# Kernel optimization log

Measured on AMD Instinct MI355X. Metric: run time of the kernel, lower is better.

The kernel has to match this reference:

```python
import jax, jax.numpy as jnp
import numpy as np

H = 512          # hidden_size of the active GRU_with_GCC
IN = 2048        # input_size of stream 1 (the encoded stream)
FS = 1536        # feats_size of stream 0 (auxiliary GCC stream)
B, T = 128, 64


def setup_inputs() -> dict:
    key = jax.random.key(0)
    ks = jax.random.split(key, 8)
    stdv = 1.0 / np.sqrt(H)
    u = lambda k, shape: jax.random.uniform(k, shape, jnp.float32, -stdv, stdv)
    return {
        "feat0": jax.random.normal(ks[0], (B, T, FS), jnp.float32),
        "feat1": jax.random.normal(ks[1], (B, T, IN), jnp.float32),
        "W_ih": u(ks[2], (3 * H, IN)),
        "b_ih": u(ks[3], (3 * H,)),
        "W_hh": u(ks[4], (3 * H, H)),
        "b_hh": u(ks[5], (3 * H,)),
        "W_fh": u(ks[6], (2 * H, FS)),
        "b_fh": u(ks[7], (2 * H,)),
    }


def reference(feat0, feat1, W_ih, b_ih, W_hh, b_hh, W_fh, b_fh):
    # Encoder_Baseline (eval mode -> dropout is identity), skip_info=[1,0]:
    # only stream 1 is encoded by GRU_with_GCC with feat0 as auxiliary gating.
    # Precompute input and auxiliary projections for all timesteps (batched GEMM).
    gi = jnp.einsum('bti,gi->btg', feat1, W_ih) + b_ih   # [B,T,3H]
    gf = jnp.einsum('btf,gf->btg', feat0, W_fh) + b_fh   # [B,T,2H]

    def step(h, inp):
        gi_t, gf_t = inp                                  # [B,3H], [B,2H]
        gh = h @ W_hh.T + b_hh                            # [B,3H]
        i_r, i_i, i_n = jnp.split(gi_t, 3, axis=-1)
        h_r, h_i, h_n = jnp.split(gh, 3, axis=-1)
        f_r, f_i = jnp.split(gf_t, 2, axis=-1)
        resetgate = jax.nn.sigmoid(i_r + h_r + f_r)
        inputgate = jax.nn.sigmoid(i_i + h_i + f_i)
        newgate = jnp.tanh(i_n + resetgate * h_n)
        hy = newgate + inputgate * (h - newgate)
        return hy, hy

    h0 = jnp.zeros((feat1.shape[0], H), feat1.dtype)
    hT, ys = jax.lax.scan(step, h0, (gi.transpose(1, 0, 2), gf.transpose(1, 0, 2)))
    eo = ys.transpose(1, 0, 2)                            # [B,T,H]
    return eo, hT
```

## Files before the change

kernel.cpp:

```cpp
#include <hip/hip_runtime.h>
#include <cstdint>
#include <cstddef>

typedef __bf16 bf16_t;
typedef bf16_t bf16x8 __attribute__((ext_vector_type(8)));
typedef float floatx4 __attribute__((ext_vector_type(4)));
typedef unsigned long long u64;

#define B_   128
#define T_   64
#define H_   512
#define IN_  2048
#define FS_  1536
#define M_   (B_ * T_)
#define GB_  64

__device__ __forceinline__ void async16(void* lds, const void* gp) {
  __builtin_amdgcn_global_load_lds(
      (const __attribute__((address_space(1))) void*)gp,
      (__attribute__((address_space(3))) void*)lds, 16, 0, 0);
}

__device__ __forceinline__ u64 cload64(const u64* p) {
  return __hip_atomic_load((u64*)p, __ATOMIC_RELAXED, __HIP_MEMORY_SCOPE_AGENT);
}
__device__ __forceinline__ void cstore64(u64* p, u64 v) {
  __hip_atomic_store(p, v, __ATOMIC_RELAXED, __HIP_MEMORY_SCOPE_AGENT);
}
__device__ __forceinline__ int cloadi(const int* p) {
  return __hip_atomic_load((int*)p, __ATOMIC_RELAXED, __HIP_MEMORY_SCOPE_AGENT);
}
__device__ __forceinline__ void cstorei(int* p, int v) {
  __hip_atomic_store(p, v, __ATOMIC_RELAXED, __HIP_MEMORY_SCOPE_AGENT);
}

__device__ __forceinline__ float fsigmoid(float x) {
  return __builtin_amdgcn_rcpf(1.f + __expf(-x));
}
__device__ __forceinline__ float ftanh(float x) {
  return 2.f * __builtin_amdgcn_rcpf(1.f + __expf(-2.f * x)) - 1.f;
}

__global__ __launch_bounds__(256) void cvt_bf16_k(const float* __restrict__ s,
                                                  bf16_t* __restrict__ d, int n8) {
  int i = blockIdx.x * 256 + threadIdx.x;
  if (i >= n8) return;
  const float4* s4 = (const float4*)s;
  float4 v0 = s4[2 * (size_t)i];
  float4 v1 = s4[2 * (size_t)i + 1];
  bf16x8 o;
  o[0] = (bf16_t)v0.x; o[1] = (bf16_t)v0.y; o[2] = (bf16_t)v0.z; o[3] = (bf16_t)v0.w;
  o[4] = (bf16_t)v1.x; o[5] = (bf16_t)v1.y; o[6] = (bf16_t)v1.z; o[7] = (bf16_t)v1.w;
  *(bf16x8*)(d + (size_t)i * 8) = o;
}

#define BM 128
#define BN 128
#define BK 32

__global__ __launch_bounds__(256) void gemm_bt_bias(
    const bf16_t* __restrict__ A, const bf16_t* __restrict__ B,
    const float* __restrict__ bias, float* __restrict__ C,
    int M, int N, int K) {
  __shared__ __align__(16) bf16_t As[BM * BK];
  __shared__ __align__(16) bf16_t Bs[BN * BK];

  const int tid  = threadIdx.x;
  const int lane = tid & 63;
  const int wave = tid >> 6;
  const int wr = wave >> 1, wc = wave & 1;
  const int mblk = blockIdx.y * BM;
  const int nblk = blockIdx.x * BN;

  const int sr = lane >> 2;
  const int sc = (lane & 3) * 8;
  const int c0 = wave * 2;

  const bf16_t* Ag0 = A + (size_t)(mblk + c0 * 16 + sr) * K + sc;
  const bf16_t* Ag1 = A + (size_t)(mblk + c0 * 16 + 16 + sr) * K + sc;
  const bf16_t* Bg0 = B + (size_t)(nblk + c0 * 16 + sr) * K + sc;
  const bf16_t* Bg1 = B + (size_t)(nblk + c0 * 16 + 16 + sr) * K + sc;
  bf16_t* As0 = As + c0 * 512;
  bf16_t* Bs0 = Bs + c0 * 512;

  floatx4 acc[4][4] = {};

  const int fm = lane & 15;
  const int fk = (lane >> 4) * 8;

  for (int kt = 0; kt < K; kt += BK) {
    async16(As0,       Ag0 + kt);
    async16(As0 + 512, Ag1 + kt);
    async16(Bs0,       Bg0 + kt);
    async16(Bs0 + 512, Bg1 + kt);
    __syncthreads();

    bf16x8 a[4], b[4];
#pragma unroll
    for (int i = 0; i < 4; i++)
      a[i] = *(const bf16x8*)(As + (wr * 64 + i * 16 + fm) * BK + fk);
#pragma unroll
    for (int j = 0; j < 4; j++)
      b[j] = *(const bf16x8*)(Bs + (wc * 64 + j * 16 + fm) * BK + fk);
#pragma unroll
    for (int i = 0; i < 4; i++)
#pragma unroll
      for (int j = 0; j < 4; j++)
        acc[i][j] = __builtin_amdgcn_mfma_f32_16x16x32_bf16(a[i], b[j], acc[i][j], 0, 0, 0);
    __syncthreads();
  }

  const int en  = nblk + wc * 64 + (lane & 15);
  const int em0 = mblk + wr * 64 + (lane >> 4) * 4;
#pragma unroll
  for (int j = 0; j < 4; j++) {
    int col = en + j * 16;
    float bv = bias[col];
#pragma unroll
    for (int i = 0; i < 4; i++) {
#pragma unroll
      for (int r = 0; r < 4; r++) {
        int row = em0 + i * 16 + r;
        C[(size_t)row * N + col] = acc[i][j][r] + bv;
      }
    }
  }
}

__global__ __launch_bounds__(256) void gru_scan(
    const float* __restrict__ Whh_f,
    const float* __restrict__ bhh,
    const float* __restrict__ gi,
    const float* __restrict__ gf,
    bf16_t* __restrict__ hbuf,
    int* __restrict__ flg,
    float* __restrict__ out) {
  __shared__ __align__(16) bf16_t wlds[48 * 64 * 8];
  __shared__ __align__(16) bf16_t swp[4][256];

  const int tid  = threadIdx.x;
  const int lane = tid & 63;
  const int w    = tid >> 6;
  const int lm   = lane & 15;
  const int lq   = lane >> 4;
  const int c    = blockIdx.x >> 1;
  const int mh   = blockIdx.x & 1;
  const int n0   = c * 16;

  for (int f = w; f < 48; f += 4) {
    int g = f >> 4, kt = f & 15;
    const float* src = Whh_f + (size_t)(g * H_ + n0 + lm) * H_ + kt * 32 + lq * 8;
    float4 v0 = *(const float4*)src;
    float4 v1 = *(const float4*)(src + 4);
    bf16x8 o;
    o[0] = (bf16_t)v0.x; o[1] = (bf16_t)v0.y; o[2] = (bf16_t)v0.z; o[3] = (bf16_t)v0.w;
    o[4] = (bf16_t)v1.x; o[5] = (bf16_t)v1.y; o[6] = (bf16_t)v1.z; o[7] = (bf16_t)v1.w;
    *(bf16x8*)(wlds + (f * 64 + lane) * 8) = o;
  }

  {
    u64* z = (u64*)(hbuf + (((size_t)mh * 32 + c) * 64 + w * 16) * 16) + lane;
    cstore64(z, 0ull);
  }
  asm volatile("s_waitcnt vmcnt(0)" ::: "memory");
  if (lane == 0) cstorei(flg + ((mh * 32 + c) * 4 + w) * 16, 1);
  __syncthreads();

  const float b0 = bhh[n0 + lm];
  const float b1 = bhh[H_ + n0 + lm];
  const float b2 = bhh[2 * H_ + n0 + lm];

  const int m0 = mh * 64 + w * 16;
  float hp[4] = {0.f, 0.f, 0.f, 0.f};

  float pir[4], pii[4], pin[4], pfr[4], pfi[4];
  auto prefetch = [&](int t) {
#pragma unroll
    for (int r = 0; r < 4; ++r) {
      size_t mrow = (size_t)(m0 + lq * 4 + r) * T_ + t;
      const float* gip = gi + mrow * (3 * H_) + n0 + lm;
      pir[r] = gip[0];
      pii[r] = gip[H_];
      pin[r] = gip[2 * H_];
      const float* gfp = gf + mrow * (2 * H_) + n0 + lm;
      pfr[r] = gfp[0];
      pfi[r] = gfp[H_];
    }
  };
  prefetch(0);

  const int* fpoll = flg + ((mh * 32 + (lane & 31)) * 4 + w) * 16;
  int* fme = flg + ((mh * 32 + c) * 4 + w) * 16;

  const size_t habase = ((size_t)mh * 32 * 64 + (size_t)w * 16 + lm) * 16 + (lq & 1) * 8;
  const size_t hct    = (size_t)(lq >> 1) * 64 * 16;

  for (int t = 0; t < T_; ++t) {
    for (;;) {
      int f = cloadi(fpoll);
      if (__all(f >= t + 1)) break;
      __builtin_amdgcn_s_sleep(1);
    }

    const bf16_t* hpar = hbuf + (size_t)(t & 1) * 65536;
    union { u64 u[2]; bf16x8 v; } a[16];
#pragma unroll
    for (int kt = 0; kt < 16; ++kt) {
      const u64* ap = (const u64*)(hpar + habase + hct + (size_t)kt * 2048);
      a[kt].u[0] = cload64(ap);
      a[kt].u[1] = cload64(ap + 1);
    }

    floatx4 acc[3] = {};
#pragma unroll
    for (int g = 0; g < 3; ++g)
#pragma unroll
      for (int kt = 0; kt < 16; ++kt) {
        bf16x8 b = *(const bf16x8*)(wlds + ((g * 16 + kt) * 64 + lane) * 8);
        acc[g] = __builtin_amdgcn_mfma_f32_16x16x32_bf16(a[kt].v, b, acc[g], 0, 0, 0);
      }

#pragma unroll
    for (int r = 0; r < 4; ++r) {
      int brow = m0 + lq * 4 + r;
      size_t mrow = (size_t)brow * T_ + t;
      float rg = fsigmoid(pir[r] + acc[0][r] + b0 + pfr[r]);
      float ig = fsigmoid(pii[r] + acc[1][r] + b1 + pfi[r]);
      float ng = ftanh(pin[r] + rg * (acc[2][r] + b2));
      float hy = ng + ig * (hp[r] - ng);
      hp[r] = hy;

      out[mrow * H_ + n0 + lm] = hy;
      if (t == T_ - 1)
        out[(size_t)M_ * H_ + (size_t)brow * H_ + n0 + lm] = hy;
      swp[w][(lq * 4 + r) * 16 + lm] = (bf16_t)hy;
    }

    if (t + 1 < T_) {
      asm volatile("s_waitcnt lgkmcnt(0)" ::: "memory");
      u64 pk = *(const u64*)(&swp[w][0] + lane * 4);
      bf16_t* hnxt = hbuf + (size_t)((t + 1) & 1) * 65536;
      u64* dst = (u64*)(hnxt + (((size_t)mh * 32 + c) * 64 + w * 16) * 16) + lane;
      cstore64(dst, pk);
      asm volatile("s_waitcnt vmcnt(0)" ::: "memory");
      if (lane == 0) cstorei(fme, t + 2);
      prefetch(t + 1);
    }
  }
}

extern "C" void kernel_launch(void* const* d_in, const int* in_sizes, int n_in,
                              void* d_out, int out_size, void* d_ws, size_t ws_size,
                              hipStream_t stream) {
  const float* feat0 = (const float*)d_in[0];
  const float* feat1 = (const float*)d_in[1];
  const float* W_ih  = (const float*)d_in[2];
  const float* b_ih  = (const float*)d_in[3];
  const float* W_hh  = (const float*)d_in[4];
  const float* b_hh  = (const float*)d_in[5];
  const float* W_fh  = (const float*)d_in[6];
  const float* b_fh  = (const float*)d_in[7];
  float* out = (float*)d_out;

  char* p = (char*)d_ws;
  int*    flg  = (int*)p;    p += 16384;
  bf16_t* hbuf = (bf16_t*)p; p += 2 * 65536 * 2;
  float*  gi   = (float*)p;  p += (size_t)M_ * 3 * H_ * 4;
  float*  gf   = (float*)p;  p += (size_t)M_ * 2 * H_ * 4;
  bf16_t* A1   = (bf16_t*)p; p += (size_t)M_ * IN_ * 2;
  bf16_t* A0   = (bf16_t*)p; p += (size_t)M_ * FS_ * 2;
  bf16_t* Wihb = (bf16_t*)p; p += (size_t)3 * H_ * IN_ * 2;
  bf16_t* Wfhb = (bf16_t*)p; p += (size_t)2 * H_ * FS_ * 2;

  hipMemsetAsync(flg, 0, 16384, stream);

  auto cvt = [&](const float* s, bf16_t* d, size_t n) {
    int n8 = (int)(n / 8);
    cvt_bf16_k<<<(n8 + 255) / 256, 256, 0, stream>>>(s, d, n8);
  };
  cvt(feat1, A1, (size_t)M_ * IN_);
  cvt(feat0, A0, (size_t)M_ * FS_);
  cvt(W_ih, Wihb, (size_t)3 * H_ * IN_);
  cvt(W_fh, Wfhb, (size_t)2 * H_ * FS_);

  gemm_bt_bias<<<dim3((3 * H_) / BN, M_ / BM), 256, 0, stream>>>(
      A1, Wihb, b_ih, gi, M_, 3 * H_, IN_);
  gemm_bt_bias<<<dim3((2 * H_) / BN, M_ / BM), 256, 0, stream>>>(
      A0, Wfhb, b_fh, gf, M_, 2 * H_, FS_);

  gru_scan<<<GB_, 256, 0, stream>>>(W_hh, b_hh, gi, gf, hbuf, flg, out);
}
```

Before: 549.8 us.

## Replace flag-based inter-block sync with sentinel-valued per-timestep hidden state buffers

```diff
diff --git a/kernel.cpp b/kernel.cpp
--- a/kernel.cpp
+++ b/kernel.cpp
@@ -14,6 +14,7 @@
 #define FS_  1536
 #define M_   (B_ * T_)
 #define GB_  64
+#define SENT (~0ull)
 
 __device__ __forceinline__ void async16(void* lds, const void* gp) {
   __builtin_amdgcn_global_load_lds(
@@ -25,12 +26,6 @@
   return __hip_atomic_load((u64*)p, __ATOMIC_RELAXED, __HIP_MEMORY_SCOPE_AGENT);
 }
 __device__ __forceinline__ void cstore64(u64* p, u64 v) {
-  __hip_atomic_store(p, v, __ATOMIC_RELAXED, __HIP_MEMORY_SCOPE_AGENT);
-}
-__device__ __forceinline__ int cloadi(const int* p) {
-  return __hip_atomic_load((int*)p, __ATOMIC_RELAXED, __HIP_MEMORY_SCOPE_AGENT);
-}
-__device__ __forceinline__ void cstorei(int* p, int v) {
   __hip_atomic_store(p, v, __ATOMIC_RELAXED, __HIP_MEMORY_SCOPE_AGENT);
 }
 
@@ -133,7 +128,6 @@
     const float* __restrict__ gi,
     const float* __restrict__ gf,
     bf16_t* __restrict__ hbuf,
-    int* __restrict__ flg,
     float* __restrict__ out) {
   __shared__ __align__(16) bf16_t wlds[48 * 64 * 8];
   __shared__ __align__(16) bf16_t swp[4][256];
@@ -162,8 +156,6 @@
     u64* z = (u64*)(hbuf + (((size_t)mh * 32 + c) * 64 + w * 16) * 16) + lane;
     cstore64(z, 0ull);
   }
-  asm volatile("s_waitcnt vmcnt(0)" ::: "memory");
-  if (lane == 0) cstorei(flg + ((mh * 32 + c) * 4 + w) * 16, 1);
   __syncthreads();
 
   const float b0 = bhh[n0 + lm];
@@ -189,26 +181,25 @@
   };
   prefetch(0);
 
-  const int* fpoll = flg + ((mh * 32 + (lane & 31)) * 4 + w) * 16;
-  int* fme = flg + ((mh * 32 + c) * 4 + w) * 16;
-
-  const size_t habase = ((size_t)mh * 32 * 64 + (size_t)w * 16 + lm) * 16 + (lq & 1) * 8;
-  const size_t hct    = (size_t)(lq >> 1) * 64 * 16;
+  const size_t habase = (size_t)mh * 32768 + ((size_t)w * 16 + lm) * 16 +
+                        (size_t)(lq >> 1) * 1024 + (lq & 1) * 8;
 
   for (int t = 0; t < T_; ++t) {
+    const bf16_t* hstep = hbuf + (size_t)t * 65536;
+    union { u64 u[2]; bf16x8 v; } a[16];
     for (;;) {
-      int f = cloadi(fpoll);
-      if (__all(f >= t + 1)) break;
+      int ok = 1;
+#pragma unroll
+      for (int kt = 0; kt < 16; ++kt) {
+        const u64* ap = (const u64*)(hstep + habase + (size_t)kt * 2048);
+        a[kt].u[0] = cload64(ap);
+        a[kt].u[1] = cload64(ap + 1);
+      }
+#pragma unroll
+      for (int kt = 0; kt < 16; ++kt)
+        ok &= (a[kt].u[0] != SENT) & (a[kt].u[1] != SENT);
+      if (__all(ok)) break;
       __builtin_amdgcn_s_sleep(1);
-    }
-
-    const bf16_t* hpar = hbuf + (size_t)(t & 1) * 65536;
-    union { u64 u[2]; bf16x8 v; } a[16];
-#pragma unroll
-    for (int kt = 0; kt < 16; ++kt) {
-      const u64* ap = (const u64*)(hpar + habase + hct + (size_t)kt * 2048);
-      a[kt].u[0] = cload64(ap);
-      a[kt].u[1] = cload64(ap + 1);
     }
 
     floatx4 acc[3] = {};
@@ -220,32 +211,34 @@
         acc[g] = __builtin_amdgcn_mfma_f32_16x16x32_bf16(a[kt].v, b, acc[g], 0, 0, 0);
       }
 
+    float hy[4];
+#pragma unroll
+    for (int r = 0; r < 4; ++r) {
+      float rg = fsigmoid(pir[r] + acc[0][r] + b0 + pfr[r]);
+      float ig = fsigmoid(pii[r] + acc[1][r] + b1 + pfi[r]);
+      float ng = ftanh(pin[r] + rg * (acc[2][r] + b2));
+      hy[r] = ng + ig * (hp[r] - ng);
+      hp[r] = hy[r];
+      swp[w][(lq * 4 + r) * 16 + lm] = (bf16_t)hy[r];
+    }
+
+    if (t + 1 < T_) {
+      asm volatile("s_waitcnt lgkmcnt(0)" ::: "memory");
+      u64 pk = *(const u64*)(&swp[w][0] + lane * 4);
+      u64* dst = (u64*)(hbuf + (size_t)(t + 1) * 65536 +
+                        (((size_t)mh * 32 + c) * 64 + w * 16) * 16) + lane;
+      cstore64(dst, pk);
+    }
+
 #pragma unroll
     for (int r = 0; r < 4; ++r) {
       int brow = m0 + lq * 4 + r;
       size_t mrow = (size_t)brow * T_ + t;
-      float rg = fsigmoid(pir[r] + acc[0][r] + b0 + pfr[r]);
-      float ig = fsigmoid(pii[r] + acc[1][r] + b1 + pfi[r]);
-      float ng = ftanh(pin[r] + rg * (acc[2][r] + b2));
-      float hy = ng + ig * (hp[r] - ng);
-      hp[r] = hy;
-
-      out[mrow * H_ + n0 + lm] = hy;
+      out[mrow * H_ + n0 + lm] = hy[r];
       if (t == T_ - 1)
-        out[(size_t)M_ * H_ + (size_t)brow * H_ + n0 + lm] = hy;
-      swp[w][(lq * 4 + r) * 16 + lm] = (bf16_t)hy;
-    }
-
-    if (t + 1 < T_) {
-      asm volatile("s_waitcnt lgkmcnt(0)" ::: "memory");
-      u64 pk = *(const u64*)(&swp[w][0] + lane * 4);
-      bf16_t* hnxt = hbuf + (size_t)((t + 1) & 1) * 65536;
-      u64* dst = (u64*)(hnxt + (((size_t)mh * 32 + c) * 64 + w * 16) * 16) + lane;
-      cstore64(dst, pk);
-      asm volatile("s_waitcnt vmcnt(0)" ::: "memory");
-      if (lane == 0) cstorei(fme, t + 2);
-      prefetch(t + 1);
-    }
+        out[(size_t)M_ * H_ + (size_t)brow * H_ + n0 + lm] = hy[r];
+    }
+    if (t + 1 < T_) prefetch(t + 1);
   }
 }
 
@@ -263,8 +256,6 @@
   float* out = (float*)d_out;
 
   char* p = (char*)d_ws;
-  int*    flg  = (int*)p;    p += 16384;
-  bf16_t* hbuf = (bf16_t*)p; p += 2 * 65536 * 2;
   float*  gi   = (float*)p;  p += (size_t)M_ * 3 * H_ * 4;
   float*  gf   = (float*)p;  p += (size_t)M_ * 2 * H_ * 4;
   bf16_t* A1   = (bf16_t*)p; p += (size_t)M_ * IN_ * 2;
@@ -272,7 +263,7 @@
   bf16_t* Wihb = (bf16_t*)p; p += (size_t)3 * H_ * IN_ * 2;
   bf16_t* Wfhb = (bf16_t*)p; p += (size_t)2 * H_ * FS_ * 2;
 
-  hipMemsetAsync(flg, 0, 16384, stream);
+  bf16_t* hbuf = A0;
 
   auto cvt = [&](const float* s, bf16_t* d, size_t n) {
     int n8 = (int)(n / 8);
@@ -288,5 +279,7 @@
   gemm_bt_bias<<<dim3((2 * H_) / BN, M_ / BM), 256, 0, stream>>>(
       A0, Wfhb, b_fh, gf, M_, 2 * H_, FS_);
 
-  gru_scan<<<GB_, 256, 0, stream>>>(W_hh, b_hh, gi, gf, hbuf, flg, out);
-}
+  hipMemsetAsync(hbuf, 0xFF, (size_t)T_ * 65536 * sizeof(bf16_t), stream);
+
+  gru_scan<<<GB_, 256, 0, stream>>>(W_hh, b_hh, gi, gf, hbuf, out);
+}
```

Result: faster. 521.5 us (-5.1%).
